# Performance work log

Hardware: AMD Instinct MI355X
Metric: run time of the kernel (lower is better)

The kernel has to match this reference:

```python
import jax, jax.numpy as jnp
import numpy as np

# FrictionConfig constants (chosen in init_kwargs)
K_STEPS = 4
ETA = 0.1
ETA_DECAY = 0.9
MU_MAX = 10.0
SMOOTH_LAMBDA = 0.1
RADIUS = 8
B, S, H = 4, 2048, 1024
INNER = max(H // 2, 32)  # 512


def _build_window_edges(length, radius):
    chunks = []
    for d in range(1, radius + 1):
        i = np.arange(length - d, dtype=np.int32)
        chunks.append(np.stack([i, i + d], axis=1))
    return np.concatenate(chunks, axis=0)  # [E, 2]


def setup_inputs() -> dict:
    key = jax.random.key(0)
    ks = jax.random.split(key, 8)
    hidden = jax.random.normal(ks[0], (B, S, H), dtype=jnp.float32)
    attention_mask = jnp.ones((B, S), dtype=jnp.int32)
    edges = jnp.asarray(_build_window_edges(S, RADIUS))
    # edge_mlp: Linear(2, INNER) -> GELU -> Linear(INNER, 1)
    W1 = jax.random.normal(ks[1], (2, INNER), dtype=jnp.float32) * (1.0 / np.sqrt(2))
    b1 = jnp.zeros((INNER,), dtype=jnp.float32)
    W2 = jax.random.normal(ks[2], (INNER, 1), dtype=jnp.float32) * (1.0 / np.sqrt(INNER))
    b2 = jnp.zeros((1,), dtype=jnp.float32)
    # q_proj: Linear(H, H)
    Wq = jax.random.normal(ks[3], (H, H), dtype=jnp.float32) * (1.0 / np.sqrt(H))
    bq = jnp.zeros((H,), dtype=jnp.float32)
    # LayerNorm
    gamma = jnp.ones((H,), dtype=jnp.float32)
    beta = jnp.zeros((H,), dtype=jnp.float32)
    return {"hidden": hidden, "attention_mask": attention_mask, "edges": edges,
            "Wq": Wq, "bq": bq, "W1": W1, "b1": b1, "W2": W2, "b2": b2,
            "gamma": gamma, "beta": beta}


def _edge_weights(h, ei, ej, W1, b1, W2, b2):
    hi = h[ei]  # [E, H]
    hj = h[ej]
    diff = hi - hj
    dist = jnp.linalg.norm(diff, axis=-1, keepdims=True)           # [E, 1]
    ni = jnp.maximum(jnp.linalg.norm(hi, axis=-1), 1e-6)
    nj = jnp.maximum(jnp.linalg.norm(hj, axis=-1), 1e-6)
    cos = (jnp.sum(hi * hj, axis=-1) / (ni * nj))[:, None]         # [E, 1]
    feats = jnp.concatenate([dist, cos], axis=-1)                  # [E, 2]
    z = jax.nn.gelu(feats @ W1 + b1, approximate=False) @ W2 + b2  # [E, 1]
    return jax.nn.softplus(z) + 1e-5


def _laplacian(h, ei, ej, mu):
    n = h.shape[0]
    weighted = mu * (h[ei] - h[ej])  # [E, H]
    # normalize_laplacian = True
    w = mu[:, 0]
    deg = jnp.zeros((n,), h.dtype).at[ei].add(w).at[ej].add(w)
    inv_sqrt = jnp.maximum(deg, 1e-6) ** -0.5
    weighted = weighted * (inv_sqrt[ei] * inv_sqrt[ej])[:, None]
    lap = jnp.zeros_like(h).at[ei].add(weighted).at[ej].add(-weighted)
    return lap


def _smooth(s):
    left = jnp.concatenate([s[:1], s[:-1]], axis=0)
    right = jnp.concatenate([s[1:], s[-1:]], axis=0)
    return s - SMOOTH_LAMBDA * (2.0 * s - left - right)


def _layernorm(x, gamma, beta):
    m = x.mean(axis=-1, keepdims=True)
    v = x.var(axis=-1, keepdims=True)
    return (x - m) * jax.lax.rsqrt(v + 1e-5) * gamma + beta


def _run_single(h, ei, ej, Wq, bq, W1, b1, W2, b2, gamma, beta):
    q = h @ Wq + bq
    state = h
    mu = None
    for step in range(K_STEPS):
        mu = _edge_weights(state, ei, ej, W1, b1, W2, b2)  # recompute_mu=True
        mu = jnp.minimum(mu, MU_MAX)
        lap = _laplacian(state, ei, ej, mu)
        eta = ETA * (ETA_DECAY ** step)
        state = state - eta * (lap - q)
        state = _smooth(state)
    out = _layernorm(state + h, gamma, beta)
    diffs = state[ei] - state[ej]
    energy = 0.5 * jnp.sum(mu[:, 0] * jnp.sum(diffs * diffs, axis=-1))
    return out, energy


def reference(hidden, attention_mask, edges, Wq, bq, W1, b1, W2, b2, gamma, beta):
    # All masks are full-length, so edges are identical across batch and
    # the outer Python batch loop vectorizes to a vmap.
    ei, ej = edges[:, 0], edges[:, 1]
    outputs, energy = jax.vmap(
        lambda h: _run_single(h, ei, ej, Wq, bq, W1, b1, W2, b2, gamma, beta)
    )(hidden)
    return outputs, energy
```

## Files before the change

kernel.cpp:

```cpp
#include <hip/hip_runtime.h>

#define BB 4
#define SS 2048
#define HH 1024
#define TQ 32
#define TU 32
#define CW 256

typedef unsigned short u16;
typedef __bf16 bf16x8 __attribute__((ext_vector_type(8)));
typedef float f32x4 __attribute__((ext_vector_type(4)));

__device__ __forceinline__ float b2f(u16 u){
  union { unsigned int i; float f; } v; v.i = ((unsigned int)u) << 16; return v.f;
}
__device__ __forceinline__ u16 f2b(float f){
  union { float f; unsigned int i; } v; v.f = f;
  unsigned int x = v.i;
  return (u16)((x + 0x7fffu + ((x >> 16) & 1u)) >> 16);
}
__device__ __forceinline__ float4 u4f(ushort4 v){
  float4 o; o.x = b2f(v.x); o.y = b2f(v.y); o.z = b2f(v.z); o.w = b2f(v.w); return o;
}
__device__ __forceinline__ ushort4 f4u(float4 v){
  ushort4 o; o.x = f2b(v.x); o.y = f2b(v.y); o.z = f2b(v.z); o.w = f2b(v.w); return o;
}
__device__ __forceinline__ float wave_sum(float v){
  #pragma unroll
  for(int m = 32; m > 0; m >>= 1) v += __shfl_xor(v, m);
  return v;
}
__device__ __forceinline__ float pread(const void* p, int i, int f){
  return f ? b2f(((const u16*)p)[i]) : ((const float*)p)[i];
}
__device__ __forceinline__ int dflag(const void* gm){
  return (((const u16*)gm)[0] == 0x3F80u) ? 1 : 0;
}
__device__ __forceinline__ void gload16(const void* g, void* l){
  __builtin_amdgcn_global_load_lds((const __attribute__((address_space(1))) unsigned int*)g,
                                   (__attribute__((address_space(3))) unsigned int*)l, 16, 0, 0);
}
__device__ __forceinline__ float  g_load(const float* p){
  return __hip_atomic_load(p, __ATOMIC_RELAXED, __HIP_MEMORY_SCOPE_AGENT);
}
__device__ __forceinline__ float  part_add(float* p, float v){
  return __hip_atomic_fetch_add(p, v, __ATOMIC_RELAXED, __HIP_MEMORY_SCOPE_AGENT);
}
__device__ __forceinline__ int    cnt_add(int* p){
  return __hip_atomic_fetch_add(p, 1, __ATOMIC_RELAXED, __HIP_MEMORY_SCOPE_AGENT);
}

__global__ __launch_bounds__(256) void k_setup(const void* hidden, u16* __restrict__ s,
                                               const void* Wq, u16* __restrict__ Wt,
                                               const void* bq, const void* W1, const void* b1,
                                               const void* W2, const void* b2, const void* gm,
                                               const void* bt,
                                               float* bqc, float* b2c, float* gmc, float* btc,
                                               float4* mlp4s, float* mkeys,
                                               float* partials, int* ecnt){
  __shared__ __align__(16) u16 t2[64][68];
  __shared__ float ka[512], kb[512], kc[512], kw[512], kk[512];
  int f = dflag(gm);
  int bid = blockIdx.x, tid = threadIdx.x;
  if(bid < 256){
    int bx = bid & 15, by = bid >> 4;
    int tx = tid & 15, ty = tid >> 4;
    #pragma unroll
    for(int rr = 0; rr < 4; rr++){
      int row = rr*16 + ty;
      size_t src = (size_t)(by*64 + row)*HH + bx*64 + tx*4;
      ushort4 v;
      if(f) v = *(const ushort4*)((const u16*)Wq + src);
      else  v = f4u(*(const float4*)((const float*)Wq + src));
      *(ushort4*)&t2[row][tx*4] = v;
    }
    __syncthreads();
    #pragma unroll
    for(int rr = 0; rr < 4; rr++){
      int n = rr*16 + ty;
      ushort4 o;
      o.x = t2[tx*4+0][n]; o.y = t2[tx*4+1][n];
      o.z = t2[tx*4+2][n]; o.w = t2[tx*4+3][n];
      *(ushort4*)(Wt + (size_t)(bx*64 + n)*HH + by*64 + tx*4) = o;
    }
  } else if(bid == 256){
    for(int i = tid; i < 1024; i += 256) bqc[i] = pread(bq, i, f);
    if(tid == 0) b2c[0] = pread(b2, 0, f);
    for(int i = tid; i < 1024; i += 256) gmc[i] = pread(gm, i, f);
    for(int i = tid; i < 1024; i += 256) btc[i] = pread(bt, i, f);
    if(tid < BB) partials[tid] = 0.f;
    if(tid == 0) ecnt[0] = 0;
    const float is2 = 0.70710678118654752f;
    for(int j = tid; j < 512; j += 256){
      float a = pread(W1, j, f)       * is2;
      float b = pread(W1, 512 + j, f) * is2;
      float c = pread(b1, j, f)       * is2;
      float w = pread(W2, j, f)       * is2;
      ka[j] = a; kb[j] = b; kc[j] = c; kw[j] = w;
      float aa = fabsf(a);
      kk[j] = (aa > 0.f) ? (4.f + fabsf(b) + fabsf(c)) * __builtin_amdgcn_rcpf(aa) : 3e38f;
    }
    __syncthreads();
    for(int j = tid; j < 512; j += 256){
      float kj = kk[j];
      int r = 0;
      for(int k = 0; k < 512; k++)
        r += (kk[k] < kj) || (kk[k] == kj && k < j);
      mlp4s[r] = make_float4(ka[j], kb[j], kc[j], kw[j]);
      mkeys[r] = kj;
    }
  } else {
    const size_t total = (size_t)BB*SS*HH/8;
    const size_t stride = (size_t)2048*256;
    size_t base = (size_t)(bid - 257)*256 + tid;
    if(f){
      for(size_t i4 = base; i4 < total; i4 += stride)
        ((uint4*)s)[i4] = ((const uint4*)hidden)[i4];
    } else {
      for(size_t i4 = base; i4 < total; i4 += stride){
        const float4* hp = (const float4*)hidden + i4*2;
        float4 v0 = hp[0], v1 = hp[1];
        ((ushort4*)s)[i4*2]   = f4u(v0);
        ((ushort4*)s)[i4*2+1] = f4u(v1);
      }
    }
  }
}

__global__ __launch_bounds__(256) void k_qgemm(const u16* __restrict__ A, const u16* __restrict__ Wt,
                                               const float* __restrict__ bqc, u16* __restrict__ q){
  __shared__ u16 lA[128*32];
  __shared__ u16 lB[128*32];
  int m0 = blockIdx.x*128, n0 = blockIdx.y*128;
  int tid  = threadIdx.x;
  int wave = tid >> 6, lane = tid & 63;
  int wm = (wave >> 1)*64, wn = (wave & 1)*64;
  int quad = lane >> 4, l16 = lane & 15;
  int srow = tid >> 2;
  int scol = (tid & 3)*8;

  f32x4 acc[4][4];
  #pragma unroll
  for(int i = 0; i < 4; i++)
    #pragma unroll
    for(int j = 0; j < 4; j++) acc[i][j] = (f32x4){0.f,0.f,0.f,0.f};

  for(int k0 = 0; k0 < HH; k0 += 32){
    __syncthreads();
    gload16(A  + (size_t)(m0 + srow     )*HH + k0 + scol, &lA[ srow     *32 + scol]);
    gload16(A  + (size_t)(m0 + srow + 64)*HH + k0 + scol, &lA[(srow+64) *32 + scol]);
    gload16(Wt + (size_t)(n0 + srow     )*HH + k0 + scol, &lB[ srow     *32 + scol]);
    gload16(Wt + (size_t)(n0 + srow + 64)*HH + k0 + scol, &lB[(srow+64) *32 + scol]);
    __syncthreads();
    bf16x8 af[4];
    #pragma unroll
    for(int mt = 0; mt < 4; mt++)
      af[mt] = *(const bf16x8*)&lA[(wm + mt*16 + l16)*32 + quad*8];
    #pragma unroll
    for(int nt = 0; nt < 4; nt++){
      bf16x8 bf = *(const bf16x8*)&lB[(wn + nt*16 + l16)*32 + quad*8];
      #pragma unroll
      for(int mt = 0; mt < 4; mt++)
        acc[mt][nt] = __builtin_amdgcn_mfma_f32_16x16x32_bf16(af[mt], bf, acc[mt][nt], 0, 0, 0);
    }
  }
  #pragma unroll
  for(int nt = 0; nt < 4; nt++){
    int col = n0 + wn + nt*16 + l16;
    float bqv = bqc[col];
    #pragma unroll
    for(int mt = 0; mt < 4; mt++){
      #pragma unroll
      for(int r = 0; r < 4; r++){
        int row = m0 + wm + mt*16 + quad*4 + r;
        q[(size_t)row*HH + col] = f2b(acc[mt][nt][r] + bqv);
      }
    }
  }
}

__device__ __forceinline__ void gram_band8(const u16* __restrict__ s, int b, int i0,
                                           float* __restrict__ Gband, int tid){
  int wave = tid >> 6, lane = tid & 63;
  if(wave < 4){
    int ti = wave >> 1;
    int tj = (wave + 1) >> 1;
    int quad = lane >> 4, l16 = lane & 15;
    int ra = i0 + ti*16 + l16; if(ra > SS-1) ra = SS-1;
    int rb = i0 + tj*16 + l16; if(rb > SS-1) rb = SS-1;
    const u16* ar = s + ((size_t)b*SS + ra)*HH + quad*8;
    const u16* br = s + ((size_t)b*SS + rb)*HH + quad*8;
    f32x4 acc0 = (f32x4){0.f,0.f,0.f,0.f};
    f32x4 acc1 = (f32x4){0.f,0.f,0.f,0.f};
    #pragma unroll 4
    for(int k0 = 0; k0 < HH; k0 += 64){
      bf16x8 a0 = *(const bf16x8*)(ar + k0);
      bf16x8 b0 = *(const bf16x8*)(br + k0);
      bf16x8 a1 = *(const bf16x8*)(ar + k0 + 32);
      bf16x8 b1 = *(const bf16x8*)(br + k0 + 32);
      acc0 = __builtin_amdgcn_mfma_f32_16x16x32_bf16(a0, b0, acc0, 0, 0, 0);
      acc1 = __builtin_amdgcn_mfma_f32_16x16x32_bf16(a1, b1, acc1, 0, 0, 0);
    }
    f32x4 acc = acc0 + acc1;
    #pragma unroll
    for(int r = 0; r < 4; r++){
      int gr = ti*16 + quad*4 + r;
      int dd = tj*16 + l16 - gr;
      if(dd >= 0 && dd <= 8) Gband[gr*9 + dd] = acc[r];
    }
  } else {
    for(int rr = wave - 4; rr < 8; rr += 4){
      int r = 32 + rr;
      int row = i0 + r; if(row > SS-1) row = SS-1;
      const ushort4* rp = (const ushort4*)(s + ((size_t)b*SS + row)*HH);
      float a = 0.f;
      #pragma unroll
      for(int c = 0; c < 4; c++){
        float4 v = u4f(rp[lane + 64*c]);
        a += v.x*v.x + v.y*v.y + v.z*v.z + v.w*v.w;
      }
      a = wave_sum(a);
      if(lane == 0) Gband[r*9] = a;
    }
  }
}

__global__ __launch_bounds__(512) void k_mu(const u16* __restrict__ s,
                                            const float4* __restrict__ mlp4s,
                                            const float* __restrict__ mkeys,
                                            const float* __restrict__ b2c,
                                            float* __restrict__ mu){
  __shared__ float Gband[40*9];
  __shared__ float4 wpk[512];
  __shared__ float skey[512];
  int b = blockIdx.y, i0 = blockIdx.x*TQ;
  int tid = threadIdx.x;
  wpk[tid] = mlp4s[tid]; skey[tid] = mkeys[tid];
  gram_band8(s, b, i0, Gband, tid);
  __syncthreads();

  int e = tid >> 1, h = tid & 1;
  int d = (e >> 5) + 1, k = e & 31;
  bool valid = (i0 + k + d) < SS;
  float gii = Gband[k*9], gjj = Gband[(k+d)*9], gij = Gband[k*9 + d];
  float dist = sqrtf(fmaxf(gii + gjj - 2.f*gij, 0.f));
  float ni = fmaxf(sqrtf(gii), 1e-6f);
  float nj = fmaxf(sqrtf(gjj), 1e-6f);
  float cosv = gij * __builtin_amdgcn_rcpf(ni * nj);
  if(!valid){ dist = 3e38f; cosv = 0.f; }

  float wmin = dist;
  #pragma unroll
  for(int m = 32; m > 0; m >>= 1) wmin = fminf(wmin, __shfl_xor(wmin, m));
  int lo = 0, hi = 512;
  while(lo < hi){ int mid = (lo + hi) >> 1; if(skey[mid] <= wmin) lo = mid + 1; else hi = mid; }
  int cut = lo - h*256; cut = (cut < 0) ? 0 : (cut > 256 ? 256 : cut);

  const float4* wp = &wpk[h*256];
  float acc = 0.f;
  int j = 0;
  #pragma unroll 4
  for(; j < cut; j++){
    float4 wv = wp[j];
    float x = fmaf(dist, wv.x, fmaf(cosv, wv.y, wv.z));
    acc = fmaf(x + fabsf(x), wv.w, acc);
  }
  #pragma unroll 2
  for(; j < 256; j++){
    float4 wv = wp[j];
    float x  = fmaf(dist, wv.x, fmaf(cosv, wv.y, wv.z));
    float ax = fabsf(x);
    float tt = __builtin_amdgcn_rcpf(fmaf(0.3275911f, ax, 1.f));
    float poly = ((((1.061405429f*tt - 1.453152027f)*tt + 1.421413741f)*tt
                   - 0.284496736f)*tt + 0.254829592f)*tt;
    float ape = ax * poly * __expf(-ax*ax);
    acc = fmaf(x + ax - ape, wv.w, acc);
  }
  acc += __shfl_xor(acc, 1);
  if(h == 0 && valid){
    float z  = acc + b2c[0];
    float sp = fmaxf(z, 0.f) + __logf(1.f + __expf(-fabsf(z)));
    mu[((size_t)b*8 + (d-1))*SS + (i0 + k)] = fminf(sp + 1e-5f, 10.0f);
  }
}

__global__ __launch_bounds__(512) void k_upsm(const u16* __restrict__ sIn, u16* __restrict__ sOut,
                                              const u16* __restrict__ q, const float* __restrict__ mu,
                                              float eta){
  __shared__ __align__(16) u16 st[50*CW];
  __shared__ float invsS[50];
  __shared__ float muS[58*8];
  int i0 = blockIdx.x*TU, c0 = blockIdx.y*CW, b = blockIdx.z;
  int tid = threadIdx.x;

  for(int idx = tid; idx < 50*(CW/8); idx += 512){
    int r = idx >> 5, cc = idx & 31;
    int i = i0 - 9 + r;
    i = (i < 0) ? 0 : ((i > SS-1) ? SS-1 : i);
    gload16(sIn + ((size_t)b*SS + i)*HH + c0 + cc*8, (uint4*)st + idx);
  }
  for(int idx = tid; idx < 58*8; idx += 512){
    int ir = idx >> 3, d = (idx & 7) + 1;
    int i = i0 - 17 + ir;
    float v = 0.f;
    if(i >= 0 && i + d < SS) v = mu[((size_t)b*8 + d-1)*SS + i];
    muS[idx] = v;
  }
  __syncthreads();
  if(tid < 50){
    int ir = tid + 8;
    float deg = 0.f;
    #pragma unroll
    for(int d = 1; d <= 8; d++){
      deg += muS[ir*8 + d-1];
      deg += muS[(ir-d)*8 + d-1];
    }
    invsS[tid] = 1.0f / sqrtf(fmaxf(deg, 1e-6f));
  }
  __syncthreads();

  int rq = tid >> 6, lane = tid & 63;
  float4 ua = {0,0,0,0}, ub = {0,0,0,0}, uc = {0,0,0,0};
  #pragma unroll
  for(int k = 0; k < 6; k++){
    int ur = rq*4 + k;
    int i  = i0 - 1 + ur;
    float4 o = {0.f,0.f,0.f,0.f};
    if(i >= 0 && i < SS){
      int sr = ur + 8, vr = ur + 8, mr = ur + 16;
      float inv_i = invsS[vr];
      float4 si = u4f(((const ushort4*)(st + (size_t)sr*CW))[lane]);
      float A = 0.f;
      float4 acc = {0.f,0.f,0.f,0.f};
      #pragma unroll
      for(int d = 1; d <= 8; d++){
        float cR = muS[mr*8 + d-1]     * inv_i        * invsS[vr+d];
        float cL = muS[(mr-d)*8 + d-1] * invsS[vr-d]  * inv_i;
        A += cR + cL;
        float4 vR = u4f(((const ushort4*)(st + (size_t)(sr+d)*CW))[lane]);
        float4 vL = u4f(((const ushort4*)(st + (size_t)(sr-d)*CW))[lane]);
        acc.x -= cR*vR.x + cL*vL.x; acc.y -= cR*vR.y + cL*vL.y;
        acc.z -= cR*vR.z + cL*vL.z; acc.w -= cR*vR.w + cL*vL.w;
      }
      acc.x += A*si.x; acc.y += A*si.y; acc.z += A*si.z; acc.w += A*si.w;
      float4 qv = u4f(*(const ushort4*)(q + ((size_t)b*SS + i)*HH + c0 + lane*4));
      o.x = si.x - eta*(acc.x - qv.x);
      o.y = si.y - eta*(acc.y - qv.y);
      o.z = si.z - eta*(acc.z - qv.z);
      o.w = si.w - eta*(acc.w - qv.w);
    }
    ua = ub; ub = uc; uc = o;
    if(k >= 2){
      int rr = rq*4 + k - 2;
      int iout = i0 + rr;
      float4 cc2 = ub;
      float4 l  = (iout > 0)     ? ua : cc2;
      float4 r4 = (iout < SS-1)  ? uc : cc2;
      float4 oo;
      oo.x = cc2.x - 0.1f*(2.f*cc2.x - l.x - r4.x);
      oo.y = cc2.y - 0.1f*(2.f*cc2.y - l.y - r4.y);
      oo.z = cc2.z - 0.1f*(2.f*cc2.z - l.z - r4.z);
      oo.w = cc2.w - 0.1f*(2.f*cc2.w - l.w - r4.w);
      *(ushort4*)(sOut + ((size_t)b*SS + iout)*HH + c0 + lane*4) = f4u(oo);
    }
  }
}

__global__ __launch_bounds__(256) void k_out(const u16* __restrict__ sA, const void* __restrict__ hraw,
                                             const float* __restrict__ gmc, const float* __restrict__ btc,
                                             void* __restrict__ outp, const void* __restrict__ gmraw){
  int f = dflag(gmraw);
  int b = blockIdx.x >> 11, i = blockIdx.x & (SS-1);
  int tid = threadIdx.x;
  size_t row = (size_t)b*SS + i;
  float4 sv = u4f(((const ushort4*)(sA + row*HH))[tid]);
  float4 hv;
  if(f) hv = u4f(((const ushort4*)((const u16*)hraw + row*HH))[tid]);
  else  hv = ((const float4*)((const float*)hraw + row*HH))[tid];
  float x0 = sv.x + hv.x, x1 = sv.y + hv.y, x2 = sv.z + hv.z, x3 = sv.w + hv.w;

  __shared__ float sh[4];
  int wv = tid >> 6, lane = tid & 63;
  float lsum = wave_sum(x0 + x1 + x2 + x3);
  if(lane == 0) sh[wv] = lsum;
  __syncthreads();
  float mean = (sh[0] + sh[1] + sh[2] + sh[3]) * (1.f/HH);
  __syncthreads();
  float d0 = x0-mean, d1 = x1-mean, d2 = x2-mean, d3 = x3-mean;
  float lsq = wave_sum(d0*d0 + d1*d1 + d2*d2 + d3*d3);
  if(lane == 0) sh[wv] = lsq;
  __syncthreads();
  float var = (sh[0] + sh[1] + sh[2] + sh[3]) * (1.f/HH);
  float sc = 1.0f / sqrtf(var + 1e-5f);

  int col = tid*4;
  float4 o;
  o.x = d0*sc*gmc[col+0] + btc[col+0];
  o.y = d1*sc*gmc[col+1] + btc[col+1];
  o.z = d2*sc*gmc[col+2] + btc[col+2];
  o.w = d3*sc*gmc[col+3] + btc[col+3];
  if(f) ((ushort4*)((u16*)outp + row*HH))[tid] = f4u(o);
  else  ((float4*)((float*)outp + row*HH))[tid] = o;
}

__global__ __launch_bounds__(512) void k_energy(const u16* __restrict__ s, const float* __restrict__ mu,
                                                float* __restrict__ partials, int* __restrict__ ecnt,
                                                void* __restrict__ outp, const void* __restrict__ gmraw){
  __shared__ float Gband[40*9];
  __shared__ float wacc[8];
  int b = blockIdx.y, i0 = blockIdx.x*TQ;
  int tid = threadIdx.x, wave = tid >> 6, lane = tid & 63;
  gram_band8(s, b, i0, Gband, tid);
  __syncthreads();

  int d = wave + 1;
  int k = lane;
  float esum = 0.f;
  if(k < 32 && (i0 + k + d) < SS){
    float d2 = fmaxf(Gband[k*9] + Gband[(k+d)*9] - 2.f*Gband[k*9 + d], 0.f);
    esum = mu[((size_t)b*8 + (d-1))*SS + (i0 + k)] * d2;
  }
  esum = wave_sum(esum);
  if(lane == 0) wacc[wave] = esum;
  __syncthreads();
  if(tid == 0){
    float t = 0.f;
    #pragma unroll
    for(int w2 = 0; w2 < 8; w2++) t += wacc[w2];
    part_add(&partials[b], t);
  }
  __syncthreads();
  if(tid == 0){
    int old = cnt_add(ecnt);
    if(old == (SS/TQ)*BB - 1){
      int f = dflag(gmraw);
      #pragma unroll
      for(int bb = 0; bb < BB; bb++){
        float e = 0.5f * g_load(&partials[bb]);
        if(f) ((u16*)outp)[(size_t)BB*SS*HH + bb] = f2b(e);
        else  ((float*)outp)[(size_t)BB*SS*HH + bb] = e;
      }
    }
  }
}

extern "C" void kernel_launch(void* const* d_in, const int* in_sizes, int n_in,
                              void* d_out, int out_size, void* d_ws, size_t ws_size,
                              hipStream_t stream) {
  const void* hidden = d_in[0];
  const void* Wq  = d_in[3];
  const void* bq  = d_in[4];
  const void* W1  = d_in[5];
  const void* b1  = d_in[6];
  const void* W2  = d_in[7];
  const void* b2v = d_in[8];
  const void* gamma = d_in[9];
  const void* beta  = d_in[10];

  char* w = (char*)d_ws;
  u16*   q   = (u16*)w;     w += (size_t)BB*SS*HH*2;
  u16*   sA  = (u16*)w;     w += (size_t)BB*SS*HH*2;
  u16*   Wt  = (u16*)w;     w += (size_t)HH*HH*2;
  float* mu  = (float*)w;   w += (size_t)BB*8*SS*4;
  float4* mlp4s = (float4*)w; w += 512*16;
  float* mkeys = (float*)w; w += 512*4;
  float* bqc = (float*)w;   w += 1024*4;
  float* b2c = (float*)w;   w += 16;
  float* gmc = (float*)w;   w += 1024*4;
  float* btc = (float*)w;   w += 1024*4;
  float* partials = (float*)w; w += 16;
  int*   ecnt = (int*)w;    w += 16;
  u16* sB = (u16*)d_out;

  k_setup<<<256 + 1 + 2048, 256, 0, stream>>>(hidden, sA, Wq, Wt, bq, W1, b1, W2, b2v,
                                              gamma, beta, bqc, b2c, gmc, btc,
                                              mlp4s, mkeys, partials, ecnt);
  k_qgemm<<<dim3(BB*SS/128, HH/128), 256, 0, stream>>>(sA, Wt, bqc, q);

  const float etas[4] = {0.1f, 0.09f, 0.081f, 0.0729f};
  for(int step = 0; step < 4; step++){
    const u16* cur = (step & 1) ? sB : sA;
    u16*       nxt = (step & 1) ? sA : sB;
    k_mu  <<<dim3(SS/TQ, BB), 512, 0, stream>>>(cur, mlp4s, mkeys, b2c, mu);
    k_upsm<<<dim3(SS/TU, HH/CW, BB), 512, 0, stream>>>(cur, nxt, q, mu, etas[step]);
  }
  k_out   <<<BB*SS, 256, 0, stream>>>(sA, hidden, gmc, btc, d_out, gamma);
  k_energy<<<dim3(SS/TQ, BB), 512, 0, stream>>>(sA, mu, partials, ecnt, d_out, gamma);
}
```

Before: 396.3 us.

## Fuse layernorm with energy kernel, remap blocks across XCDs, precompute Laplacian coefficients

New measurement: 369.6 us. -6.7%, faster.

```diff
diff --git a/kernel.cpp b/kernel.cpp
--- a/kernel.cpp
+++ b/kernel.cpp
@@ -30,6 +30,7 @@
   for(int m = 32; m > 0; m >>= 1) v += __shfl_xor(v, m);
   return v;
 }
+__device__ __forceinline__ float sumf4(float4 a){ return (a.x + a.y) + (a.z + a.w); }
 __device__ __forceinline__ float pread(const void* p, int i, int f){
   return f ? b2f(((const u16*)p)[i]) : ((const float*)p)[i];
 }
@@ -233,7 +234,9 @@
   __shared__ float Gband[40*9];
   __shared__ float4 wpk[512];
   __shared__ float skey[512];
-  int b = blockIdx.y, i0 = blockIdx.x*TQ;
+  int L = blockIdx.x + 64*blockIdx.y;
+  int V = (L & 7)*32 + (L >> 3);
+  int b = V >> 6, i0 = (V & 63)*TQ;
   int tid = threadIdx.x;
   wpk[tid] = mlp4s[tid]; skey[tid] = mkeys[tid];
   gram_band8(s, b, i0, Gband, tid);
@@ -287,17 +290,22 @@
 __global__ __launch_bounds__(512) void k_upsm(const u16* __restrict__ sIn, u16* __restrict__ sOut,
                                               const u16* __restrict__ q, const float* __restrict__ mu,
                                               float eta){
-  __shared__ __align__(16) u16 st[50*CW];
+  __shared__ u16 st[50*CW];
   __shared__ float invsS[50];
   __shared__ float muS[58*8];
-  int i0 = blockIdx.x*TU, c0 = blockIdx.y*CW, b = blockIdx.z;
+  __shared__ float cRS[34*8];
+  __shared__ float cLS[34*8];
+  int L = blockIdx.x + 64*(blockIdx.y + 4*blockIdx.z);
+  int V = (L & 7)*128 + (L >> 3);
+  int i0 = (V & 63)*TU, c0 = ((V >> 6) & 3)*CW, b = V >> 8;
   int tid = threadIdx.x;
 
   for(int idx = tid; idx < 50*(CW/8); idx += 512){
     int r = idx >> 5, cc = idx & 31;
     int i = i0 - 9 + r;
-    i = (i < 0) ? 0 : ((i > SS-1) ? SS-1 : i);
-    gload16(sIn + ((size_t)b*SS + i)*HH + c0 + cc*8, (uint4*)st + idx);
+    uint4 v = {0,0,0,0};
+    if(i >= 0 && i < SS) v = *(const uint4*)(sIn + ((size_t)b*SS + i)*HH + c0 + cc*8);
+    ((uint4*)st)[idx] = v;
   }
   for(int idx = tid; idx < 58*8; idx += 512){
     int ir = idx >> 3, d = (idx & 7) + 1;
@@ -316,6 +324,13 @@
       deg += muS[(ir-d)*8 + d-1];
     }
     invsS[tid] = 1.0f / sqrtf(fmaxf(deg, 1e-6f));
+  }
+  __syncthreads();
+  if(tid < 272){
+    int ur = tid >> 3, d = (tid & 7) + 1;
+    int vr = ur + 8, mr = ur + 16;
+    cRS[tid] = muS[mr*8 + d-1]     * invsS[vr]   * invsS[vr+d];
+    cLS[tid] = muS[(mr-d)*8 + d-1] * invsS[vr-d] * invsS[vr];
   }
   __syncthreads();
 
@@ -327,15 +342,14 @@
     int i  = i0 - 1 + ur;
     float4 o = {0.f,0.f,0.f,0.f};
     if(i >= 0 && i < SS){
-      int sr = ur + 8, vr = ur + 8, mr = ur + 16;
-      float inv_i = invsS[vr];
+      int sr = ur + 8;
       float4 si = u4f(((const ushort4*)(st + (size_t)sr*CW))[lane]);
       float A = 0.f;
       float4 acc = {0.f,0.f,0.f,0.f};
       #pragma unroll
       for(int d = 1; d <= 8; d++){
-        float cR = muS[mr*8 + d-1]     * inv_i        * invsS[vr+d];
-        float cL = muS[(mr-d)*8 + d-1] * invsS[vr-d]  * inv_i;
+        float cR = cRS[ur*8 + d-1];
+        float cL = cLS[ur*8 + d-1];
         A += cR + cL;
         float4 vR = u4f(((const ushort4*)(st + (size_t)(sr+d)*CW))[lane]);
         float4 vL = u4f(((const ushort4*)(st + (size_t)(sr-d)*CW))[lane]);
@@ -366,62 +380,30 @@
   }
 }
 
-__global__ __launch_bounds__(256) void k_out(const u16* __restrict__ sA, const void* __restrict__ hraw,
+__global__ __launch_bounds__(512) void k_fin(const u16* __restrict__ s, const float* __restrict__ mu,
+                                             float* __restrict__ partials, int* __restrict__ ecnt,
+                                             const void* __restrict__ hidden,
                                              const float* __restrict__ gmc, const float* __restrict__ btc,
                                              void* __restrict__ outp, const void* __restrict__ gmraw){
-  int f = dflag(gmraw);
-  int b = blockIdx.x >> 11, i = blockIdx.x & (SS-1);
-  int tid = threadIdx.x;
-  size_t row = (size_t)b*SS + i;
-  float4 sv = u4f(((const ushort4*)(sA + row*HH))[tid]);
-  float4 hv;
-  if(f) hv = u4f(((const ushort4*)((const u16*)hraw + row*HH))[tid]);
-  else  hv = ((const float4*)((const float*)hraw + row*HH))[tid];
-  float x0 = sv.x + hv.x, x1 = sv.y + hv.y, x2 = sv.z + hv.z, x3 = sv.w + hv.w;
-
-  __shared__ float sh[4];
-  int wv = tid >> 6, lane = tid & 63;
-  float lsum = wave_sum(x0 + x1 + x2 + x3);
-  if(lane == 0) sh[wv] = lsum;
-  __syncthreads();
-  float mean = (sh[0] + sh[1] + sh[2] + sh[3]) * (1.f/HH);
-  __syncthreads();
-  float d0 = x0-mean, d1 = x1-mean, d2 = x2-mean, d3 = x3-mean;
-  float lsq = wave_sum(d0*d0 + d1*d1 + d2*d2 + d3*d3);
-  if(lane == 0) sh[wv] = lsq;
-  __syncthreads();
-  float var = (sh[0] + sh[1] + sh[2] + sh[3]) * (1.f/HH);
-  float sc = 1.0f / sqrtf(var + 1e-5f);
-
-  int col = tid*4;
-  float4 o;
-  o.x = d0*sc*gmc[col+0] + btc[col+0];
-  o.y = d1*sc*gmc[col+1] + btc[col+1];
-  o.z = d2*sc*gmc[col+2] + btc[col+2];
-  o.w = d3*sc*gmc[col+3] + btc[col+3];
-  if(f) ((ushort4*)((u16*)outp + row*HH))[tid] = f4u(o);
-  else  ((float4*)((float*)outp + row*HH))[tid] = o;
-}
-
-__global__ __launch_bounds__(512) void k_energy(const u16* __restrict__ s, const float* __restrict__ mu,
-                                                float* __restrict__ partials, int* __restrict__ ecnt,
-                                                void* __restrict__ outp, const void* __restrict__ gmraw){
   __shared__ float Gband[40*9];
   __shared__ float wacc[8];
-  int b = blockIdx.y, i0 = blockIdx.x*TQ;
+  int L = blockIdx.x + 64*blockIdx.y;
+  int V = (L & 7)*32 + (L >> 3);
+  int b = V >> 6, i0 = (V & 63)*TQ;
   int tid = threadIdx.x, wave = tid >> 6, lane = tid & 63;
   gram_band8(s, b, i0, Gband, tid);
   __syncthreads();
 
-  int d = wave + 1;
-  int k = lane;
-  float esum = 0.f;
-  if(k < 32 && (i0 + k + d) < SS){
-    float d2 = fmaxf(Gband[k*9] + Gband[(k+d)*9] - 2.f*Gband[k*9 + d], 0.f);
-    esum = mu[((size_t)b*8 + (d-1))*SS + (i0 + k)] * d2;
-  }
-  esum = wave_sum(esum);
-  if(lane == 0) wacc[wave] = esum;
+  {
+    int d = wave + 1;
+    float esum = 0.f;
+    if(lane < 32 && (i0 + lane + d) < SS){
+      float d2 = fmaxf(Gband[lane*9] + Gband[(lane+d)*9] - 2.f*Gband[lane*9 + d], 0.f);
+      esum = mu[((size_t)b*8 + (d-1))*SS + (i0 + lane)] * d2;
+    }
+    esum = wave_sum(esum);
+    if(lane == 0) wacc[wave] = esum;
+  }
   __syncthreads();
   if(tid == 0){
     float t = 0.f;
@@ -429,11 +411,62 @@
     for(int w2 = 0; w2 < 8; w2++) t += wacc[w2];
     part_add(&partials[b], t);
   }
+
+  int f = dflag(gmraw);
+  const float4* gmp = (const float4*)(gmc + (size_t)lane*16);
+  const float4* btp = (const float4*)(btc + (size_t)lane*16);
+  float4 g0 = gmp[0], g1 = gmp[1], g2 = gmp[2], g3 = gmp[3];
+  float4 t0 = btp[0], t1 = btp[1], t2 = btp[2], t3 = btp[3];
+  #pragma unroll
+  for(int j = 0; j < 4; j++){
+    int i = i0 + wave*4 + j;
+    size_t row = (size_t)b*SS + i;
+    const ushort4* sp = (const ushort4*)(s + row*HH + (size_t)lane*16);
+    float4 x0 = u4f(sp[0]), x1 = u4f(sp[1]), x2 = u4f(sp[2]), x3 = u4f(sp[3]);
+    if(f){
+      const ushort4* hp = (const ushort4*)((const u16*)hidden + row*HH + (size_t)lane*16);
+      float4 h0 = u4f(hp[0]), h1 = u4f(hp[1]), h2 = u4f(hp[2]), h3 = u4f(hp[3]);
+      x0.x+=h0.x; x0.y+=h0.y; x0.z+=h0.z; x0.w+=h0.w;
+      x1.x+=h1.x; x1.y+=h1.y; x1.z+=h1.z; x1.w+=h1.w;
+      x2.x+=h2.x; x2.y+=h2.y; x2.z+=h2.z; x2.w+=h2.w;
+      x3.x+=h3.x; x3.y+=h3.y; x3.z+=h3.z; x3.w+=h3.w;
+    } else {
+      const float4* hp = (const float4*)((const float*)hidden + row*HH + (size_t)lane*16);
+      float4 h0 = hp[0], h1 = hp[1], h2 = hp[2], h3 = hp[3];
+      x0.x+=h0.x; x0.y+=h0.y; x0.z+=h0.z; x0.w+=h0.w;
+      x1.x+=h1.x; x1.y+=h1.y; x1.z+=h1.z; x1.w+=h1.w;
+      x2.x+=h2.x; x2.y+=h2.y; x2.z+=h2.z; x2.w+=h2.w;
+      x3.x+=h3.x; x3.y+=h3.y; x3.z+=h3.z; x3.w+=h3.w;
+    }
+    float mean = wave_sum((sumf4(x0)+sumf4(x1))+(sumf4(x2)+sumf4(x3))) * (1.f/HH);
+    x0.x-=mean; x0.y-=mean; x0.z-=mean; x0.w-=mean;
+    x1.x-=mean; x1.y-=mean; x1.z-=mean; x1.w-=mean;
+    x2.x-=mean; x2.y-=mean; x2.z-=mean; x2.w-=mean;
+    x3.x-=mean; x3.y-=mean; x3.z-=mean; x3.w-=mean;
+    float sq = (x0.x*x0.x+x0.y*x0.y+x0.z*x0.z+x0.w*x0.w)
+             + (x1.x*x1.x+x1.y*x1.y+x1.z*x1.z+x1.w*x1.w)
+             + (x2.x*x2.x+x2.y*x2.y+x2.z*x2.z+x2.w*x2.w)
+             + (x3.x*x3.x+x3.y*x3.y+x3.z*x3.z+x3.w*x3.w);
+    float var = wave_sum(sq) * (1.f/HH);
+    float sc = 1.0f / sqrtf(var + 1e-5f);
+    float4 o0, o1, o2, o3;
+    o0.x = x0.x*sc*g0.x + t0.x; o0.y = x0.y*sc*g0.y + t0.y; o0.z = x0.z*sc*g0.z + t0.z; o0.w = x0.w*sc*g0.w + t0.w;
+    o1.x = x1.x*sc*g1.x + t1.x; o1.y = x1.y*sc*g1.y + t1.y; o1.z = x1.z*sc*g1.z + t1.z; o1.w = x1.w*sc*g1.w + t1.w;
+    o2.x = x2.x*sc*g2.x + t2.x; o2.y = x2.y*sc*g2.y + t2.y; o2.z = x2.z*sc*g2.z + t2.z; o2.w = x2.w*sc*g2.w + t2.w;
+    o3.x = x3.x*sc*g3.x + t3.x; o3.y = x3.y*sc*g3.y + t3.y; o3.z = x3.z*sc*g3.z + t3.z; o3.w = x3.w*sc*g3.w + t3.w;
+    if(f){
+      ushort4* op = (ushort4*)((u16*)outp + row*HH + (size_t)lane*16);
+      op[0] = f4u(o0); op[1] = f4u(o1); op[2] = f4u(o2); op[3] = f4u(o3);
+    } else {
+      float4* op = (float4*)((float*)outp + row*HH + (size_t)lane*16);
+      op[0] = o0; op[1] = o1; op[2] = o2; op[3] = o3;
+    }
+  }
+
   __syncthreads();
   if(tid == 0){
     int old = cnt_add(ecnt);
-    if(old == (SS/TQ)*BB - 1){
-      int f = dflag(gmraw);
+    if(old == 64*BB - 1){
       #pragma unroll
       for(int bb = 0; bb < BB; bb++){
         float e = 0.5f * g_load(&partials[bb]);
@@ -484,6 +517,5 @@
     k_mu  <<<dim3(SS/TQ, BB), 512, 0, stream>>>(cur, mlp4s, mkeys, b2c, mu);
     k_upsm<<<dim3(SS/TU, HH/CW, BB), 512, 0, stream>>>(cur, nxt, q, mu, etas[step]);
   }
-  k_out   <<<BB*SS, 256, 0, stream>>>(sA, hidden, gmc, btc, d_out, gamma);
-  k_energy<<<dim3(SS/TQ, BB), 512, 0, stream>>>(sA, mu, partials, ecnt, d_out, gamma);
-}
+  k_fin<<<dim3(SS/TQ, BB), 512, 0, stream>>>(sA, mu, partials, ecnt, hidden, gmc, btc, d_out, gamma);
+}
```
